# Kernel tuning notes

Hardware: AMD Instinct MI355X
Metric: run time of the kernel (lower is better)

## Reference

```python
import jax, jax.numpy as jnp
import numpy as np

B, C, H, W = 4, 384, 248, 216
NUM_ANCHORS = 6           # len(rotations)=2 * len(sizes)=3
NUM_CLASSES = 3
BOX_CODE_SIZE = 7
CLS_OUT = NUM_ANCHORS * NUM_CLASSES      # 18
REG_OUT = NUM_ANCHORS * BOX_CODE_SIZE    # 42
DIR_OUT = NUM_ANCHORS * 2                # 12


def setup_inputs() -> dict:
    key = jax.random.key(0)
    ks = jax.random.split(key, 4)
    x = jax.random.normal(ks[0], (B, C, H, W), dtype=jnp.float32)
    scale = 0.02
    w_cls = jax.random.normal(ks[1], (C, CLS_OUT), dtype=jnp.float32) * scale
    w_reg = jax.random.normal(ks[2], (C, REG_OUT), dtype=jnp.float32) * scale
    w_dir = jax.random.normal(ks[3], (C, DIR_OUT), dtype=jnp.float32) * scale
    b_cls = jnp.zeros((CLS_OUT,), dtype=jnp.float32)
    b_reg = jnp.zeros((REG_OUT,), dtype=jnp.float32)
    b_dir = jnp.zeros((DIR_OUT,), dtype=jnp.float32)
    return {"x": x, "w_cls": w_cls, "b_cls": b_cls, "w_reg": w_reg,
            "b_reg": b_reg, "w_dir": w_dir, "b_dir": b_dir}


def _conv1x1(x, w, b):
    # channels_first 1x1 conv == per-pixel matmul over channels
    return jnp.einsum('bchw,co->bohw', x, w) + b[None, :, None, None]


def reference(x, w_cls, b_cls, w_reg, b_reg, w_dir, b_dir):
    cls_score = _conv1x1(x, w_cls, b_cls)      # [B, 18, H, W]
    bbox_pred = _conv1x1(x, w_reg, b_reg)      # [B, 42, H, W]
    dir_cls_preds = _conv1x1(x, w_dir, b_dir)  # [B, 12, H, W]
    return (cls_score, bbox_pred, dir_cls_preds)
```

## Files before the change

### kernel.cpp

```cpp
#include <hip/hip_runtime.h>


constexpr int Bn   = 4;
constexpr int Cc   = 384;
constexpr int Hh   = 248;
constexpr int Ww   = 216;
constexpr int HW   = Hh * Ww;
constexpr int NPIX = Bn * HW;
constexpr int NCLS = 18;
constexpr int NREG = 42;
constexpr int NDIR = 12;

template<int NA, int LDA, int NB, int LDB>
__device__ __forceinline__ void cohort_run(
    const float* __restrict__ xb,
    const float* __restrict__ wA, const float* __restrict__ bA,
    float* __restrict__ oA,
    const float* __restrict__ wB, const float* __restrict__ bB,
    float* __restrict__ oB)
{
    float acc[NA + NB];
    #pragma unroll
    for (int j = 0; j < NA; ++j) acc[j] = bA[j];
    #pragma unroll
    for (int j = 0; j < NB; ++j) acc[NA + j] = bB[j];

    #pragma unroll 4
    for (int c = 0; c < Cc; ++c) {
        const float xv = xb[(size_t)c * HW];
        #pragma unroll
        for (int j = 0; j < NA; ++j)
            acc[j] = fmaf(xv, wA[c * LDA + j], acc[j]);
        #pragma unroll
        for (int j = 0; j < NB; ++j)
            acc[NA + j] = fmaf(xv, wB[c * LDB + j], acc[NA + j]);
    }

    #pragma unroll
    for (int j = 0; j < NA; ++j) oA[(size_t)j * HW] = acc[j];
    #pragma unroll
    for (int j = 0; j < NB; ++j) oB[(size_t)j * HW] = acc[NA + j];
}

__global__ __launch_bounds__(256) void head_fused_msplit(
    const float* __restrict__ x,
    const float* __restrict__ wc, const float* __restrict__ bc,
    const float* __restrict__ wr, const float* __restrict__ br,
    const float* __restrict__ wd, const float* __restrict__ bd,
    float* __restrict__ out)
{
    const int w    = threadIdx.x >> 6;
    const int lane = threadIdx.x & 63;
    const int pix  = blockIdx.x * 64 + lane;
    const int b    = pix / HW;
    const int p    = pix - b * HW;

    const float* __restrict__ xb = x + (size_t)b * Cc * HW + p;

    float* __restrict__ outc = out + (size_t)b * NCLS * HW + p;
    float* __restrict__ outr = out + (size_t)Bn * NCLS * HW
                                   + (size_t)b * NREG * HW + p;
    float* __restrict__ outd = out + (size_t)Bn * (NCLS + NREG) * HW
                                   + (size_t)b * NDIR * HW + p;

    if (w == 0) {
        cohort_run<18, NCLS, 0, 1>(xb, wc, bc, outc, wc, bc, outc);
    } else if (w == 1) {
        cohort_run<18, NREG, 0, 1>(xb, wr, br, outr, wr, br, outr);
    } else if (w == 2) {
        cohort_run<18, NREG, 0, 1>(xb, wr + 18, br + 18, outr + (size_t)18 * HW,
                                   wr, br, outr);
    } else {
        cohort_run<6, NREG, 12, NDIR>(xb, wr + 36, br + 36, outr + (size_t)36 * HW,
                                      wd, bd, outd);
    }
}

extern "C" void kernel_launch(void* const* d_in, const int* in_sizes, int n_in,
                              void* d_out, int out_size, void* d_ws, size_t ws_size,
                              hipStream_t stream) {
    const float* x  = (const float*)d_in[0];
    const float* wc = (const float*)d_in[1];
    const float* bc = (const float*)d_in[2];
    const float* wr = (const float*)d_in[3];
    const float* br = (const float*)d_in[4];
    const float* wd = (const float*)d_in[5];
    const float* bd = (const float*)d_in[6];
    float* out = (float*)d_out;

    dim3 grid(NPIX / 64);
    dim3 block(256);
    head_fused_msplit<<<grid, block, 0, stream>>>(x, wc, bc, wr, br, wd, bd, out);
}
```

Measured before the change: 531.1 us.

## Double-buffer channel loads in registers, add nontemporal stores and occupancy hint

Restructures the channel loop into chunks of 8 with two register buffers, so the loads for later channels are issued before the FMAs on the current chunk, hiding global-load latency. Output stores become nontemporal to avoid polluting cache, and launch bounds request 6 blocks per SM. The extra buffers raise register pressure, and the occupancy hint may force spills.

```diff
diff --git a/kernel.cpp b/kernel.cpp
--- a/kernel.cpp
+++ b/kernel.cpp
@@ -10,6 +10,7 @@
 constexpr int NCLS = 18;
 constexpr int NREG = 42;
 constexpr int NDIR = 12;
+constexpr int CH   = 8;
 
 template<int NA, int LDA, int NB, int LDB>
 __device__ __forceinline__ void cohort_run(
@@ -19,30 +20,67 @@
     const float* __restrict__ wB, const float* __restrict__ bB,
     float* __restrict__ oB)
 {
-    float acc[NA + NB];
+    constexpr int NO = NA + NB;
+    float acc[NO];
     #pragma unroll
     for (int j = 0; j < NA; ++j) acc[j] = bA[j];
     #pragma unroll
     for (int j = 0; j < NB; ++j) acc[NA + j] = bB[j];
 
-    #pragma unroll 4
-    for (int c = 0; c < Cc; ++c) {
-        const float xv = xb[(size_t)c * HW];
+    float bufA[CH], bufB[CH];
+    #pragma unroll
+    for (int i = 0; i < CH; ++i) bufA[i] = xb[(size_t)i * HW];
+    #pragma unroll
+    for (int i = 0; i < CH; ++i) bufB[i] = xb[(size_t)(CH + i) * HW];
+
+    for (int c0 = 0; c0 < Cc; c0 += 2 * CH) {
+        float xt[CH];
         #pragma unroll
-        for (int j = 0; j < NA; ++j)
-            acc[j] = fmaf(xv, wA[c * LDA + j], acc[j]);
+        for (int i = 0; i < CH; ++i) xt[i] = bufA[i];
+        if (c0 + 2 * CH < Cc) {
+            #pragma unroll
+            for (int i = 0; i < CH; ++i)
+                bufA[i] = xb[(size_t)(c0 + 2 * CH + i) * HW];
+        }
+        asm volatile("" ::: "memory");
         #pragma unroll
-        for (int j = 0; j < NB; ++j)
-            acc[NA + j] = fmaf(xv, wB[c * LDB + j], acc[NA + j]);
+        for (int i = 0; i < CH; ++i) {
+            const float* __restrict__ wra = wA + (size_t)(c0 + i) * LDA;
+            const float* __restrict__ wrb = wB + (size_t)(c0 + i) * LDB;
+            #pragma unroll
+            for (int j = 0; j < NA; ++j) acc[j]      = fmaf(xt[i], wra[j], acc[j]);
+            #pragma unroll
+            for (int j = 0; j < NB; ++j) acc[NA + j] = fmaf(xt[i], wrb[j], acc[NA + j]);
+        }
+
+        #pragma unroll
+        for (int i = 0; i < CH; ++i) xt[i] = bufB[i];
+        if (c0 + 3 * CH < Cc) {
+            #pragma unroll
+            for (int i = 0; i < CH; ++i)
+                bufB[i] = xb[(size_t)(c0 + 3 * CH + i) * HW];
+        }
+        asm volatile("" ::: "memory");
+        #pragma unroll
+        for (int i = 0; i < CH; ++i) {
+            const float* __restrict__ wra = wA + (size_t)(c0 + CH + i) * LDA;
+            const float* __restrict__ wrb = wB + (size_t)(c0 + CH + i) * LDB;
+            #pragma unroll
+            for (int j = 0; j < NA; ++j) acc[j]      = fmaf(xt[i], wra[j], acc[j]);
+            #pragma unroll
+            for (int j = 0; j < NB; ++j) acc[NA + j] = fmaf(xt[i], wrb[j], acc[NA + j]);
+        }
     }
 
     #pragma unroll
-    for (int j = 0; j < NA; ++j) oA[(size_t)j * HW] = acc[j];
+    for (int j = 0; j < NA; ++j)
+        __builtin_nontemporal_store(acc[j], oA + (size_t)j * HW);
     #pragma unroll
-    for (int j = 0; j < NB; ++j) oB[(size_t)j * HW] = acc[NA + j];
+    for (int j = 0; j < NB; ++j)
+        __builtin_nontemporal_store(acc[NA + j], oB + (size_t)j * HW);
 }
 
-__global__ __launch_bounds__(256) void head_fused_msplit(
+__global__ __launch_bounds__(256, 6) void head_fused_pf(
     const float* __restrict__ x,
     const float* __restrict__ wc, const float* __restrict__ bc,
     const float* __restrict__ wr, const float* __restrict__ br,
@@ -90,5 +128,5 @@
 
     dim3 grid(NPIX / 64);
     dim3 block(256);
-    head_fused_msplit<<<grid, block, 0, stream>>>(x, wc, bc, wr, br, wd, bd, out);
+    head_fused_pf<<<grid, block, 0, stream>>>(x, wc, bc, wr, br, wd, bd, out);
 }
```

Result: slower. 574.8 us (+8.2%).

## Stage input channels in LDS via async global-to-LDS triple buffering

Applied to the files above, without the earlier changes.

Each of the four waves previously read the same 64-pixel slice of x from global memory on its own. Now the block cooperatively stages 16-channel chunks into a 3-deep LDS ring using global_load_lds. Explicit vmcnt waits and barriers overlap the next chunk's load with the FMAs on the current one. This removes the 4x redundant global reads of x, at the cost of per-chunk barriers and inline asm waitcnt handling.

```diff
diff --git a/kernel.cpp b/kernel.cpp
--- a/kernel.cpp
+++ b/kernel.cpp
@@ -1,4 +1,5 @@
 #include <hip/hip_runtime.h>
+#include <cstdint>
 
 
 constexpr int Bn   = 4;
@@ -10,24 +11,20 @@
 constexpr int NCLS = 18;
 constexpr int NREG = 42;
 constexpr int NDIR = 12;
+constexpr int CH     = 16;
+constexpr int NCHUNK = Cc / CH;
+
+typedef const __attribute__((address_space(1))) void* as1cp;
+typedef __attribute__((address_space(3))) void*       as3p;
 
 template<int NA, int LDA, int NB, int LDB>
-__device__ __forceinline__ void cohort_run(
-    const float* __restrict__ xb,
-    const float* __restrict__ wA, const float* __restrict__ bA,
-    float* __restrict__ oA,
-    const float* __restrict__ wB, const float* __restrict__ bB,
-    float* __restrict__ oB)
+__device__ __forceinline__ void chunk_fma(
+    float (&acc)[18], const float (*xc)[64], const int lane,
+    const float* __restrict__ wA, const float* __restrict__ wB)
 {
-    float acc[NA + NB];
     #pragma unroll
-    for (int j = 0; j < NA; ++j) acc[j] = bA[j];
-    #pragma unroll
-    for (int j = 0; j < NB; ++j) acc[NA + j] = bB[j];
-
-    #pragma unroll 4
-    for (int c = 0; c < Cc; ++c) {
-        const float xv = xb[(size_t)c * HW];
+    for (int c = 0; c < CH; ++c) {
+        const float xv = xc[c][lane];
         #pragma unroll
         for (int j = 0; j < NA; ++j)
             acc[j] = fmaf(xv, wA[c * LDA + j], acc[j]);
@@ -35,44 +32,105 @@
         for (int j = 0; j < NB; ++j)
             acc[NA + j] = fmaf(xv, wB[c * LDB + j], acc[NA + j]);
     }
-
-    #pragma unroll
-    for (int j = 0; j < NA; ++j) oA[(size_t)j * HW] = acc[j];
-    #pragma unroll
-    for (int j = 0; j < NB; ++j) oB[(size_t)j * HW] = acc[NA + j];
 }
 
-__global__ __launch_bounds__(256) void head_fused_msplit(
+__global__ __launch_bounds__(256) void head_fused_lds(
     const float* __restrict__ x,
     const float* __restrict__ wc, const float* __restrict__ bc,
     const float* __restrict__ wr, const float* __restrict__ br,
     const float* __restrict__ wd, const float* __restrict__ bd,
     float* __restrict__ out)
 {
+    __shared__ float xs[3][CH][64];
+
     const int w    = threadIdx.x >> 6;
     const int lane = threadIdx.x & 63;
-    const int pix  = blockIdx.x * 64 + lane;
-    const int b    = pix / HW;
-    const int p    = pix - b * HW;
+    const int w4   = w << 2;
+    const int pb   = blockIdx.x * 64;
+    const int b    = pb / HW;
+    const int p    = pb - b * HW;
 
-    const float* __restrict__ xb = x + (size_t)b * Cc * HW + p;
+    const float* xrow = x + (size_t)b * Cc * HW + p;
+    const float* xg   = xrow + (size_t)(w4 + (lane >> 4)) * HW + (lane & 15) * 4;
 
-    float* __restrict__ outc = out + (size_t)b * NCLS * HW + p;
-    float* __restrict__ outr = out + (size_t)Bn * NCLS * HW
-                                   + (size_t)b * NREG * HW + p;
-    float* __restrict__ outd = out + (size_t)Bn * (NCLS + NREG) * HW
-                                   + (size_t)b * NDIR * HW + p;
+    float* outc = out + (size_t)b * NCLS * HW + p + lane;
+    float* outr = out + (size_t)Bn * NCLS * HW + (size_t)b * NREG * HW + p + lane;
+    float* outd = out + (size_t)Bn * (NCLS + NREG) * HW
+                      + (size_t)b * NDIR * HW + p + lane;
+
+    float acc[18];
+    if (w == 0) {
+        #pragma unroll
+        for (int j = 0; j < 18; ++j) acc[j] = bc[j];
+    } else if (w == 1) {
+        #pragma unroll
+        for (int j = 0; j < 18; ++j) acc[j] = br[j];
+    } else if (w == 2) {
+        #pragma unroll
+        for (int j = 0; j < 18; ++j) acc[j] = br[18 + j];
+    } else {
+        #pragma unroll
+        for (int j = 0; j < 6; ++j)  acc[j] = br[36 + j];
+        #pragma unroll
+        for (int j = 0; j < 12; ++j) acc[6 + j] = bd[j];
+    }
+
+    __builtin_amdgcn_global_load_lds((as1cp)xg,
+                                     (as3p)&xs[0][w4][0], 16, 0, 0);
+    __builtin_amdgcn_global_load_lds((as1cp)(xg + (size_t)CH * HW),
+                                     (as3p)&xs[1][w4][0], 16, 0, 0);
+
+    int bs = 0;
+    #pragma unroll 1
+    for (int t = 0; t < NCHUNK; ++t) {
+        if (t + 2 < NCHUNK) {
+            const int bf = (bs + 2 >= 3) ? bs - 1 : bs + 2;
+            __builtin_amdgcn_global_load_lds(
+                (as1cp)(xg + (size_t)(t + 2) * CH * HW),
+                (as3p)&xs[bf][w4][0], 16, 0, 0);
+            asm volatile("s_waitcnt vmcnt(2)" ::: "memory");
+        } else if (t + 2 == NCHUNK) {
+            asm volatile("s_waitcnt vmcnt(1)" ::: "memory");
+        } else {
+            asm volatile("s_waitcnt vmcnt(0)" ::: "memory");
+        }
+        __builtin_amdgcn_s_barrier();
+
+        const float* xc0 = &xs[bs][0][0];
+        const float (*xc)[64] = (const float (*)[64])xc0;
+        if (w == 0) {
+            chunk_fma<18, NCLS, 0, 1>(acc, xc, lane,
+                                      wc + (size_t)t * CH * NCLS, wc);
+        } else if (w == 1) {
+            chunk_fma<18, NREG, 0, 1>(acc, xc, lane,
+                                      wr + (size_t)t * CH * NREG, wr);
+        } else if (w == 2) {
+            chunk_fma<18, NREG, 0, 1>(acc, xc, lane,
+                                      wr + 18 + (size_t)t * CH * NREG, wr);
+        } else {
+            chunk_fma<6, NREG, 12, NDIR>(acc, xc, lane,
+                                         wr + 36 + (size_t)t * CH * NREG,
+                                         wd + (size_t)t * CH * NDIR);
+        }
+
+        if (t + 1 < NCHUNK) __builtin_amdgcn_s_barrier();
+        bs = (bs + 1 == 3) ? 0 : bs + 1;
+    }
 
     if (w == 0) {
-        cohort_run<18, NCLS, 0, 1>(xb, wc, bc, outc, wc, bc, outc);
+        #pragma unroll
+        for (int j = 0; j < 18; ++j) outc[(size_t)j * HW] = acc[j];
     } else if (w == 1) {
-        cohort_run<18, NREG, 0, 1>(xb, wr, br, outr, wr, br, outr);
+        #pragma unroll
+        for (int j = 0; j < 18; ++j) outr[(size_t)j * HW] = acc[j];
     } else if (w == 2) {
-        cohort_run<18, NREG, 0, 1>(xb, wr + 18, br + 18, outr + (size_t)18 * HW,
-                                   wr, br, outr);
+        #pragma unroll
+        for (int j = 0; j < 18; ++j) outr[(size_t)(18 + j) * HW] = acc[j];
     } else {
-        cohort_run<6, NREG, 12, NDIR>(xb, wr + 36, br + 36, outr + (size_t)36 * HW,
-                                      wd, bd, outd);
+        #pragma unroll
+        for (int j = 0; j < 6; ++j)  outr[(size_t)(36 + j) * HW] = acc[j];
+        #pragma unroll
+        for (int j = 0; j < 12; ++j) outd[(size_t)j * HW] = acc[6 + j];
     }
 }
 
@@ -90,5 +148,5 @@
 
     dim3 grid(NPIX / 64);
     dim3 block(256);
-    head_fused_msplit<<<grid, block, 0, stream>>>(x, wc, bc, wr, br, wd, bd, out);
+    head_fused_lds<<<grid, block, 0, stream>>>(x, wc, bc, wr, br, wd, bd, out);
 }
```

Measured after the change: 654.8 us. 1.23x slower.
